# Kernel optimization log

Measured on AMD Instinct MI355X. Metric: run time of the kernel, lower is better.

Reference implementation:

```python
import jax, jax.numpy as jnp
import numpy as np

COMMITMENT_COST = 0.25
ENTROPY_LOSS_WEIGHT = 0.1
EPSILON = 1e-05
NUM_EMBEDDINGS = 2048
EMBEDDING_DIM = 64


def setup_inputs() -> dict:
    key = jax.random.key(0)
    kx, ke = jax.random.split(key)
    x = jax.random.normal(kx, (16, 64, 64, EMBEDDING_DIM), dtype=jnp.float32)
    embedding = jax.random.normal(ke, (NUM_EMBEDDINGS, EMBEDDING_DIM), dtype=jnp.float32)
    return {"x": x, "embedding": embedding}


def reference(x, embedding):
    input_shape = x.shape
    flat_x = x.reshape(-1, EMBEDDING_DIM)              # [N, D]
    distances = (jnp.sum(flat_x ** 2, axis=1, keepdims=True)
                 + jnp.sum(embedding ** 2, axis=1)
                 - 2.0 * jnp.matmul(flat_x, embedding.T))
    encoding_indices = jnp.argmin(distances, axis=1)   # [N]
    quantized = embedding[encoding_indices].reshape(input_shape)

    commitment_loss = jnp.mean((jax.lax.stop_gradient(quantized) - x) ** 2)
    codebook_loss = jnp.mean((quantized - jax.lax.stop_gradient(x)) ** 2)
    # straight-through estimator
    quantized = x + jax.lax.stop_gradient(quantized - x)

    # histogram of code usage == mean of one-hot encodings (scatter-add, avoids [N,K] one-hot)
    n_tokens = flat_x.shape[0]
    counts = jnp.zeros((NUM_EMBEDDINGS,), dtype=flat_x.dtype).at[encoding_indices].add(1.0)
    avg_probs = counts / n_tokens
    perplexity = jnp.exp(-jnp.sum(avg_probs * jnp.log(avg_probs + EPSILON)))
    entropy_loss = jnp.sum(avg_probs * jnp.log(avg_probs + EPSILON))

    vq_loss = codebook_loss + COMMITMENT_COST * commitment_loss + ENTROPY_LOSS_WEIGHT * entropy_loss
    return (quantized, vq_loss, commitment_loss, codebook_loss, perplexity,
            entropy_loss, encoding_indices.reshape(input_shape[:-1]), avg_probs)
```

## Files before the change

kernel.cpp:

```cpp
#include <hip/hip_runtime.h>
#include <float.h>

typedef _Float16 half8 __attribute__((ext_vector_type(8)));
typedef float    f32x4 __attribute__((ext_vector_type(4)));

constexpr int N_TOK = 65536;
constexpr int D     = 64;
constexpr int K     = 2048;
constexpr int TILE_C = 64;
constexpr int NTILE  = K / TILE_C;
constexpr int TOK_PER_BLK = 64;
constexpr int NBLK = N_TOK / TOK_PER_BLK;
constexpr float EPS_RESCORE = 2e-3f;

constexpr size_t QN       = (size_t)N_TOK * D;
constexpr size_t SCAL_OFF = QN;
constexpr size_t IDX_OFF  = QN + 5;
constexpr size_t PROB_OFF = IDX_OFF + N_TOK;

constexpr size_t WS_HNORM = 0;
constexpr size_t WS_COUNT = 8192;
constexpr size_t WS_BSUM  = 16384;
constexpr size_t WS_SW    = 24576;

__device__ inline unsigned long long pack_key(float d, int k) {
    unsigned u = __float_as_uint(d);
    u = (u & 0x80000000u) ? ~u : (u | 0x80000000u);
    return ((unsigned long long)u << 32) | (unsigned)k;
}

__device__ inline float unpack_dist(unsigned long long key) {
    unsigned u = (unsigned)(key >> 32);
    u = (u & 0x80000000u) ? (u & 0x7FFFFFFFu) : ~u;
    return __uint_as_float(u);
}

__device__ inline unsigned long long shfl_xor_u64_w16(unsigned long long v, int m) {
    int lo = __shfl_xor((int)(unsigned)v, m, 16);
    int hi = __shfl_xor((int)(unsigned)(v >> 32), m, 16);
    return ((unsigned long long)(unsigned)hi << 32) | (unsigned)lo;
}

__global__ __launch_bounds__(256) void vq_init(const float* __restrict__ emb,
                                               float* __restrict__ hnorm,
                                               unsigned* __restrict__ counts,
                                               double* __restrict__ blocksums,
                                               half8* __restrict__ sw) {
    const int g  = blockIdx.x * 256 + threadIdx.x;
    const int r  = g >> 3;
    const int c0 = g & 7;
    const float4* p4 = (const float4*)(emb + (size_t)r * D + 8 * c0);
    float4 q0 = p4[0], q1 = p4[1];
    float v[8] = {q0.x, q0.y, q0.z, q0.w, q1.x, q1.y, q1.z, q1.w};
    half8 h, l;
    float s = 0.f;
#pragma unroll
    for (int i = 0; i < 8; ++i) {
        s += v[i] * v[i];
        _Float16 hh = (_Float16)v[i];
        h[i] = hh;
        l[i] = (_Float16)(v[i] - (float)hh);
    }
    const int t    = r >> 6;
    const int w    = (r >> 4) & 3;
    const int m16  = r & 15;
    const int lane = (c0 & 3) * 16 + m16;
    const int slot = c0 >> 2;
    half8* dst = sw + ((size_t)((t * 4 + w) * 64 + lane)) * 4;
    dst[slot]     = h;
    dst[2 + slot] = l;

#pragma unroll
    for (int off = 1; off < 8; off <<= 1) s += __shfl_xor(s, off, 8);
    if (c0 == 0) hnorm[r] = 0.5f * s;
    if (g < K) counts[g] = 0u;
    if (g < NBLK) blocksums[g] = 0.0;
}

#define VQ_STEP(B0, B1, B2, B3, HN, CODE)                                          \
  {                                                                                \
    _Pragma("unroll")                                                              \
    for (int a = 0; a < 4; ++a) {                                                  \
      f32x4 acc = {(HN), (HN), (HN), (HN)};                                        \
      acc = __builtin_amdgcn_mfma_f32_16x16x32_f16(axh[a][0], (B0), acc, 0, 0, 0); \
      acc = __builtin_amdgcn_mfma_f32_16x16x32_f16(axh[a][1], (B1), acc, 0, 0, 0); \
      acc = __builtin_amdgcn_mfma_f32_16x16x32_f16(axl[a][0], (B0), acc, 0, 0, 0); \
      acc = __builtin_amdgcn_mfma_f32_16x16x32_f16(axl[a][1], (B1), acc, 0, 0, 0); \
      acc = __builtin_amdgcn_mfma_f32_16x16x32_f16(axh[a][0], (B2), acc, 0, 0, 0); \
      acc = __builtin_amdgcn_mfma_f32_16x16x32_f16(axh[a][1], (B3), acc, 0, 0, 0); \
      _Pragma("unroll")                                                            \
      for (int r = 0; r < 4; ++r)                                                  \
        if (acc[r] < best_d[a][r]) { best_d[a][r] = acc[r]; best_k[a][r] = (CODE); } \
    }                                                                              \
  }

__global__ __launch_bounds__(256) void vq_fused(const float* __restrict__ x,
                                                const float* __restrict__ emb,
                                                const float* __restrict__ hnorm,
                                                const half8* __restrict__ sw,
                                                unsigned* __restrict__ counts,
                                                double* __restrict__ blocksums,
                                                float* __restrict__ out) {
    __shared__ unsigned long long kls[64][5];
    __shared__ int bks[64];
    __shared__ double wsum[4];

    const int tid  = threadIdx.x;
    const int lane = tid & 63;
    const int wav  = tid >> 6;
    const int t0   = blockIdx.x * TOK_PER_BLK;
    const int m16  = lane & 15;
    const int g    = lane >> 4;
    const int ko   = g * 8;
    const int cit  = wav * 16 + m16;

    half8 axh[4][2], axl[4][2];
#pragma unroll
    for (int a = 0; a < 4; ++a) {
        const float* xr = x + (size_t)(t0 + 16 * a + m16) * D;
#pragma unroll
        for (int c = 0; c < 2; ++c) {
            const float4* p4 = (const float4*)(xr + 32 * c + ko);
            float4 q0 = p4[0], q1 = p4[1];
            float v[8] = {q0.x, q0.y, q0.z, q0.w, q1.x, q1.y, q1.z, q1.w};
            half8 h, l;
#pragma unroll
            for (int j = 0; j < 8; ++j) {
                float nv = -v[j];
                _Float16 hh = (_Float16)nv;
                h[j] = hh;
                l[j] = (_Float16)(nv - (float)hh);
            }
            axh[a][c] = h; axl[a][c] = l;
        }
    }

    float best_d[4][4];
    int   best_k[4][4];
#pragma unroll
    for (int a = 0; a < 4; ++a)
#pragma unroll
        for (int r = 0; r < 4; ++r) { best_d[a][r] = FLT_MAX; best_k[a][r] = 0; }

    const half8* pb = sw + (size_t)tid * 4;
    const float* ph = hnorm + cit;
    int code = cit;

    half8 e0 = pb[0], e1 = pb[1], e2 = pb[2], e3 = pb[3];
    float eh = *ph;

    for (int t = 0; t < NTILE; t += 2) {
        const half8* po = pb + 1024;
        half8 o0 = po[0], o1 = po[1], o2 = po[2], o3 = po[3];
        float oh = ph[64];

        VQ_STEP(e0, e1, e2, e3, eh, code);
        code += 64;

        if (t + 2 < NTILE) {
            pb += 2048; ph += 128;
            e0 = pb[0]; e1 = pb[1]; e2 = pb[2]; e3 = pb[3];
            eh = *ph;
        }

        VQ_STEP(o0, o1, o2, o3, oh, code);
        code += 64;
    }

#pragma unroll
    for (int a = 0; a < 4; ++a)
#pragma unroll
        for (int r = 0; r < 4; ++r) {
            unsigned long long key = pack_key(best_d[a][r], best_k[a][r]);
#pragma unroll
            for (int off = 8; off; off >>= 1) {
                unsigned long long o = shfl_xor_u64_w16(key, off);
                if (o < key) key = o;
            }
            if (m16 == 0) kls[16 * a + g * 4 + r][wav] = key;
        }
    __syncthreads();

    if (tid < 64) {
        float ds[4]; int kk[4];
        unsigned long long kmin = ~0ULL;
#pragma unroll
        for (int w = 0; w < 4; ++w) {
            unsigned long long key = kls[tid][w];
            ds[w] = unpack_dist(key);
            kk[w] = (int)(unsigned)(key & 0xFFFFFFFFu);
            if (key < kmin) kmin = key;
        }
        int bk = (int)(unsigned)(kmin & 0xFFFFFFFFu);
        const float fmin = unpack_dist(kmin);
        int cnt = 0;
#pragma unroll
        for (int w = 0; w < 4; ++w) cnt += (ds[w] <= fmin + EPS_RESCORE) ? 1 : 0;

        if (cnt > 1) {
            unsigned long long bkey = ~0ULL;
            const float* xr = x + (size_t)(t0 + tid) * D;
            for (int w = 0; w < 4; ++w) {
                if (ds[w] <= fmin + EPS_RESCORE) {
                    const int k = kk[w];
                    const float* cr = emb + (size_t)k * D;
                    float s0 = 0.f, s1 = 0.f, s2 = 0.f, s3 = 0.f;
#pragma unroll
                    for (int i = 0; i < 16; ++i) {
                        s0 = fmaf(cr[4 * i + 0], xr[4 * i + 0], s0);
                        s1 = fmaf(cr[4 * i + 1], xr[4 * i + 1], s1);
                        s2 = fmaf(cr[4 * i + 2], xr[4 * i + 2], s2);
                        s3 = fmaf(cr[4 * i + 3], xr[4 * i + 3], s3);
                    }
                    float hd = hnorm[k] - ((s0 + s1) + (s2 + s3));
                    unsigned long long key = pack_key(hd, k);
                    if (key < bkey) bkey = key;
                }
            }
            bk = (int)(unsigned)(bkey & 0xFFFFFFFFu);
        }
        bks[tid] = bk;
        out[IDX_OFF + t0 + tid] = (float)bk;
        atomicAdd(&counts[bk], 1u);
    }
    __syncthreads();

    const int tok = tid >> 2;
    const int i4  = tid & 3;
    const int bk  = bks[tok];
    const float4* xr4 = (const float4*)(x + (size_t)(t0 + tok) * D);
    const float4* cr4 = (const float4*)(emb + (size_t)bk * D);
    float4* qr4 = (float4*)(out + (size_t)(t0 + tok) * D);
    float local = 0.f;
#pragma unroll
    for (int ii = 0; ii < 4; ++ii) {
        const int idx = i4 + 4 * ii;
        float4 xv = xr4[idx];
        float4 cv = cr4[idx];
        float dx = cv.x - xv.x, dy = cv.y - xv.y;
        float dz = cv.z - xv.z, dw = cv.w - xv.w;
        local += dx * dx + dy * dy + dz * dz + dw * dw;
        float4 q;
        q.x = xv.x + dx; q.y = xv.y + dy;
        q.z = xv.z + dz; q.w = xv.w + dw;
        qr4[idx] = q;
    }
    double ld = (double)local;
#pragma unroll
    for (int off = 32; off > 0; off >>= 1) ld += __shfl_down(ld, off, 64);
    if (lane == 0) wsum[wav] = ld;
    __syncthreads();
    if (tid == 0)
        blocksums[blockIdx.x] = (wsum[0] + wsum[1]) + (wsum[2] + wsum[3]);
}

__global__ __launch_bounds__(256) void vq_finalize(const unsigned* __restrict__ counts,
                                                   const double* __restrict__ blocksums,
                                                   float* __restrict__ out) {
    const int tid = threadIdx.x;
    double e = 0.0;
#pragma unroll
    for (int i = 0; i < 8; ++i) {
        int k = tid + i * 256;
        float p = (float)counts[k] / 65536.0f;
        out[PROB_OFF + k] = p;
        double pd = (double)p;
        e += pd * log(pd + 1e-5);
    }
    double s = 0.0;
#pragma unroll
    for (int i = 0; i < NBLK / 256; ++i) s += blocksums[tid + i * 256];
#pragma unroll
    for (int off = 32; off > 0; off >>= 1) {
        e += __shfl_down(e, off, 64);
        s += __shfl_down(s, off, 64);
    }
    __shared__ double we[4], ws2[4];
    int lane = tid & 63, wid = tid >> 6;
    if (lane == 0) { we[wid] = e; ws2[wid] = s; }
    __syncthreads();
    if (tid == 0) {
        double entropy = (we[0] + we[1]) + (we[2] + we[3]);
        double sumsq   = (ws2[0] + ws2[1]) + (ws2[2] + ws2[3]);
        double mse     = sumsq / (double)((size_t)N_TOK * D);
        out[SCAL_OFF + 0] = (float)(1.25 * mse + 0.1 * entropy);
        out[SCAL_OFF + 1] = (float)mse;
        out[SCAL_OFF + 2] = (float)mse;
        out[SCAL_OFF + 3] = (float)exp(-entropy);
        out[SCAL_OFF + 4] = (float)entropy;
    }
}

extern "C" void kernel_launch(void* const* d_in, const int* in_sizes, int n_in,
                              void* d_out, int out_size, void* d_ws, size_t ws_size,
                              hipStream_t stream) {
    const float* x   = (const float*)d_in[0];
    const float* emb = (const float*)d_in[1];
    float* out = (float*)d_out;

    char* ws = (char*)d_ws;
    float*    hnorm     = (float*)(ws + WS_HNORM);
    unsigned* counts    = (unsigned*)(ws + WS_COUNT);
    double*   blocksums = (double*)(ws + WS_BSUM);
    half8*    sw        = (half8*)(ws + WS_SW);

    vq_init<<<K * 8 / 256, 256, 0, stream>>>(emb, hnorm, counts, blocksums, sw);
    vq_fused<<<NBLK, 256, 0, stream>>>(x, emb, hnorm, sw, counts, blocksums, out);
    vq_finalize<<<1, 256, 0, stream>>>(counts, blocksums, out);
}
```

Baseline: 134.4 us.

## Split codebook search across two blocks per token group with ticket merge

```diff
diff --git a/kernel.cpp b/kernel.cpp
--- a/kernel.cpp
+++ b/kernel.cpp
@@ -8,9 +8,10 @@
 constexpr int D     = 64;
 constexpr int K     = 2048;
 constexpr int TILE_C = 64;
-constexpr int NTILE  = K / TILE_C;
+constexpr int NTILE_H = 16;
 constexpr int TOK_PER_BLK = 64;
-constexpr int NBLK = N_TOK / TOK_PER_BLK;
+constexpr int NGRP = N_TOK / TOK_PER_BLK;
+constexpr int NBLK = NGRP * 2;
 constexpr float EPS_RESCORE = 2e-3f;
 
 constexpr size_t QN       = (size_t)N_TOK * D;
@@ -21,7 +22,9 @@
 constexpr size_t WS_HNORM = 0;
 constexpr size_t WS_COUNT = 8192;
 constexpr size_t WS_BSUM  = 16384;
-constexpr size_t WS_SW    = 24576;
+constexpr size_t WS_TICK  = 24576;
+constexpr size_t WS_KEYS  = 28672;
+constexpr size_t WS_SW    = 28672 + (size_t)2 * N_TOK * 8;
 
 __device__ inline unsigned long long pack_key(float d, int k) {
     unsigned u = __float_as_uint(d);
@@ -44,7 +47,7 @@
 __global__ __launch_bounds__(256) void vq_init(const float* __restrict__ emb,
                                                float* __restrict__ hnorm,
                                                unsigned* __restrict__ counts,
-                                               double* __restrict__ blocksums,
+                                               unsigned* __restrict__ ticket,
                                                half8* __restrict__ sw) {
     const int g  = blockIdx.x * 256 + threadIdx.x;
     const int r  = g >> 3;
@@ -66,7 +69,7 @@
     const int m16  = r & 15;
     const int lane = (c0 & 3) * 16 + m16;
     const int slot = c0 >> 2;
-    half8* dst = sw + ((size_t)((t * 4 + w) * 64 + lane)) * 4;
+    half8* dst = sw + ((size_t)(t * 256 + w * 64 + lane)) * 4;
     dst[slot]     = h;
     dst[2 + slot] = l;
 
@@ -74,7 +77,7 @@
     for (int off = 1; off < 8; off <<= 1) s += __shfl_xor(s, off, 8);
     if (c0 == 0) hnorm[r] = 0.5f * s;
     if (g < K) counts[g] = 0u;
-    if (g < NBLK) blocksums[g] = 0.0;
+    if (g < NGRP) ticket[g] = 0u;
 }
 
 #define VQ_STEP(B0, B1, B2, B3, HN, CODE)                                          \
@@ -99,20 +102,26 @@
                                                 const float* __restrict__ hnorm,
                                                 const half8* __restrict__ sw,
                                                 unsigned* __restrict__ counts,
+                                                unsigned* __restrict__ ticket,
+                                                unsigned long long* __restrict__ keys,
                                                 double* __restrict__ blocksums,
                                                 float* __restrict__ out) {
     __shared__ unsigned long long kls[64][5];
     __shared__ int bks[64];
     __shared__ double wsum[4];
+    __shared__ int is_last_s;
 
     const int tid  = threadIdx.x;
     const int lane = tid & 63;
     const int wav  = tid >> 6;
-    const int t0   = blockIdx.x * TOK_PER_BLK;
+    const int grp  = blockIdx.x >> 1;
+    const int half = blockIdx.x & 1;
+    const int t0   = grp * TOK_PER_BLK;
     const int m16  = lane & 15;
     const int g    = lane >> 4;
     const int ko   = g * 8;
     const int cit  = wav * 16 + m16;
+    const int cbase = half * (K / 2);
 
     half8 axh[4][2], axl[4][2];
 #pragma unroll
@@ -142,14 +151,14 @@
 #pragma unroll
         for (int r = 0; r < 4; ++r) { best_d[a][r] = FLT_MAX; best_k[a][r] = 0; }
 
-    const half8* pb = sw + (size_t)tid * 4;
-    const float* ph = hnorm + cit;
-    int code = cit;
+    const half8* pb = sw + ((size_t)(half * NTILE_H) * 256 + tid) * 4;
+    const float* ph = hnorm + cbase + cit;
+    int code = cbase + cit;
 
     half8 e0 = pb[0], e1 = pb[1], e2 = pb[2], e3 = pb[3];
     float eh = *ph;
 
-    for (int t = 0; t < NTILE; t += 2) {
+    for (int t = 0; t < NTILE_H; t += 2) {
         const half8* po = pb + 1024;
         half8 o0 = po[0], o1 = po[1], o2 = po[2], o3 = po[3];
         float oh = ph[64];
@@ -157,7 +166,7 @@
         VQ_STEP(e0, e1, e2, e3, eh, code);
         code += 64;
 
-        if (t + 2 < NTILE) {
+        if (t + 2 < NTILE_H) {
             pb += 2048; ph += 128;
             e0 = pb[0]; e1 = pb[1]; e2 = pb[2]; e3 = pb[3];
             eh = *ph;
@@ -191,7 +200,6 @@
             kk[w] = (int)(unsigned)(key & 0xFFFFFFFFu);
             if (key < kmin) kmin = key;
         }
-        int bk = (int)(unsigned)(kmin & 0xFFFFFFFFu);
         const float fmin = unpack_dist(kmin);
         int cnt = 0;
 #pragma unroll
@@ -217,10 +225,52 @@
                     if (key < bkey) bkey = key;
                 }
             }
+            kmin = bkey;
+        }
+        keys[(size_t)half * N_TOK + t0 + tid] = kmin;
+        __threadfence();
+    }
+    __syncthreads();
+    if (tid == 0)
+        is_last_s = (atomicAdd(&ticket[grp], 1u) == 1u);
+    __syncthreads();
+    if (!is_last_s) return;
+    __threadfence();
+
+    if (tid < 64) {
+        const int tok = t0 + tid;
+        unsigned long long k0 = keys[tok];
+        unsigned long long k1 = keys[(size_t)N_TOK + tok];
+        float d0 = unpack_dist(k0), d1 = unpack_dist(k1);
+        unsigned long long kmin = (k0 < k1) ? k0 : k1;
+        int bk = (int)(unsigned)(kmin & 0xFFFFFFFFu);
+        const float fmin = unpack_dist(kmin);
+
+        if (d0 <= fmin + EPS_RESCORE && d1 <= fmin + EPS_RESCORE) {
+            unsigned long long bkey = ~0ULL;
+            const float* xr = x + (size_t)tok * D;
+            const int cand[2] = {(int)(unsigned)(k0 & 0xFFFFFFFFu),
+                                 (int)(unsigned)(k1 & 0xFFFFFFFFu)};
+#pragma unroll
+            for (int w = 0; w < 2; ++w) {
+                const int k = cand[w];
+                const float* cr = emb + (size_t)k * D;
+                float s0 = 0.f, s1 = 0.f, s2 = 0.f, s3 = 0.f;
+#pragma unroll
+                for (int i = 0; i < 16; ++i) {
+                    s0 = fmaf(cr[4 * i + 0], xr[4 * i + 0], s0);
+                    s1 = fmaf(cr[4 * i + 1], xr[4 * i + 1], s1);
+                    s2 = fmaf(cr[4 * i + 2], xr[4 * i + 2], s2);
+                    s3 = fmaf(cr[4 * i + 3], xr[4 * i + 3], s3);
+                }
+                float hd = hnorm[k] - ((s0 + s1) + (s2 + s3));
+                unsigned long long key = pack_key(hd, k);
+                if (key < bkey) bkey = key;
+            }
             bk = (int)(unsigned)(bkey & 0xFFFFFFFFu);
         }
         bks[tid] = bk;
-        out[IDX_OFF + t0 + tid] = (float)bk;
+        out[IDX_OFF + tok] = (float)bk;
         atomicAdd(&counts[bk], 1u);
     }
     __syncthreads();
@@ -251,7 +301,7 @@
     if (lane == 0) wsum[wav] = ld;
     __syncthreads();
     if (tid == 0)
-        blocksums[blockIdx.x] = (wsum[0] + wsum[1]) + (wsum[2] + wsum[3]);
+        blocksums[grp] = (wsum[0] + wsum[1]) + (wsum[2] + wsum[3]);
 }
 
 __global__ __launch_bounds__(256) void vq_finalize(const unsigned* __restrict__ counts,
@@ -269,7 +319,7 @@
     }
     double s = 0.0;
 #pragma unroll
-    for (int i = 0; i < NBLK / 256; ++i) s += blocksums[tid + i * 256];
+    for (int i = 0; i < NGRP / 256; ++i) s += blocksums[tid + i * 256];
 #pragma unroll
     for (int off = 32; off > 0; off >>= 1) {
         e += __shfl_down(e, off, 64);
@@ -302,9 +352,12 @@
     float*    hnorm     = (float*)(ws + WS_HNORM);
     unsigned* counts    = (unsigned*)(ws + WS_COUNT);
     double*   blocksums = (double*)(ws + WS_BSUM);
+    unsigned* ticket    = (unsigned*)(ws + WS_TICK);
+    unsigned long long* keys = (unsigned long long*)(ws + WS_KEYS);
     half8*    sw        = (half8*)(ws + WS_SW);
 
-    vq_init<<<K * 8 / 256, 256, 0, stream>>>(emb, hnorm, counts, blocksums, sw);
-    vq_fused<<<NBLK, 256, 0, stream>>>(x, emb, hnorm, sw, counts, blocksums, out);
+    vq_init<<<K * 8 / 256, 256, 0, stream>>>(emb, hnorm, counts, ticket, sw);
+    vq_fused<<<NBLK, 256, 0, stream>>>(x, emb, hnorm, sw, counts, ticket, keys,
+                                       blocksums, out);
     vq_finalize<<<1, 256, 0, stream>>>(counts, blocksums, out);
 }
```

Result: slower. 360.4 us (+168.1%).

## Deepen codebook prefetch to two tiles ahead and batch MFMAs under raised priority

Applied to the files above, without the earlier changes.

```diff
diff --git a/kernel.cpp b/kernel.cpp
--- a/kernel.cpp
+++ b/kernel.cpp
@@ -66,7 +66,7 @@
     const int m16  = r & 15;
     const int lane = (c0 & 3) * 16 + m16;
     const int slot = c0 >> 2;
-    half8* dst = sw + ((size_t)((t * 4 + w) * 64 + lane)) * 4;
+    half8* dst = sw + ((size_t)(t * 256 + w * 64 + lane)) * 4;
     dst[slot]     = h;
     dst[2 + slot] = l;
 
@@ -77,30 +77,42 @@
     if (g < NBLK) blocksums[g] = 0.0;
 }
 
-#define VQ_STEP(B0, B1, B2, B3, HN, CODE)                                          \
+#define LOADB(TOFF, B, HN)                                                         \
   {                                                                                \
+    const half8* _q = pb + (TOFF) * 1024;                                          \
+    B##0 = _q[0]; B##1 = _q[1]; B##2 = _q[2]; B##3 = _q[3];                        \
+    HN = ph[(TOFF) * 64];                                                          \
+  }
+
+#define VQ_STEP(B, HN, CODE)                                                       \
+  {                                                                                \
+    f32x4 acc[4];                                                                  \
+    __builtin_amdgcn_s_setprio(1);                                                 \
     _Pragma("unroll")                                                              \
     for (int a = 0; a < 4; ++a) {                                                  \
-      f32x4 acc = {(HN), (HN), (HN), (HN)};                                        \
-      acc = __builtin_amdgcn_mfma_f32_16x16x32_f16(axh[a][0], (B0), acc, 0, 0, 0); \
-      acc = __builtin_amdgcn_mfma_f32_16x16x32_f16(axh[a][1], (B1), acc, 0, 0, 0); \
-      acc = __builtin_amdgcn_mfma_f32_16x16x32_f16(axl[a][0], (B0), acc, 0, 0, 0); \
-      acc = __builtin_amdgcn_mfma_f32_16x16x32_f16(axl[a][1], (B1), acc, 0, 0, 0); \
-      acc = __builtin_amdgcn_mfma_f32_16x16x32_f16(axh[a][0], (B2), acc, 0, 0, 0); \
-      acc = __builtin_amdgcn_mfma_f32_16x16x32_f16(axh[a][1], (B3), acc, 0, 0, 0); \
+      acc[a] = (f32x4){(HN), (HN), (HN), (HN)};                                    \
+      acc[a] = __builtin_amdgcn_mfma_f32_16x16x32_f16(axh[a][0], B##0, acc[a], 0, 0, 0); \
+      acc[a] = __builtin_amdgcn_mfma_f32_16x16x32_f16(axh[a][1], B##1, acc[a], 0, 0, 0); \
+      acc[a] = __builtin_amdgcn_mfma_f32_16x16x32_f16(axl[a][0], B##0, acc[a], 0, 0, 0); \
+      acc[a] = __builtin_amdgcn_mfma_f32_16x16x32_f16(axl[a][1], B##1, acc[a], 0, 0, 0); \
+      acc[a] = __builtin_amdgcn_mfma_f32_16x16x32_f16(axh[a][0], B##2, acc[a], 0, 0, 0); \
+      acc[a] = __builtin_amdgcn_mfma_f32_16x16x32_f16(axh[a][1], B##3, acc[a], 0, 0, 0); \
+    }                                                                              \
+    __builtin_amdgcn_s_setprio(0);                                                 \
+    _Pragma("unroll")                                                              \
+    for (int a = 0; a < 4; ++a)                                                    \
       _Pragma("unroll")                                                            \
       for (int r = 0; r < 4; ++r)                                                  \
-        if (acc[r] < best_d[a][r]) { best_d[a][r] = acc[r]; best_k[a][r] = (CODE); } \
-    }                                                                              \
+        if (acc[a][r] < best_d[a][r]) { best_d[a][r] = acc[a][r]; best_k[a][r] = (CODE); } \
   }
 
-__global__ __launch_bounds__(256) void vq_fused(const float* __restrict__ x,
-                                                const float* __restrict__ emb,
-                                                const float* __restrict__ hnorm,
-                                                const half8* __restrict__ sw,
-                                                unsigned* __restrict__ counts,
-                                                double* __restrict__ blocksums,
-                                                float* __restrict__ out) {
+__global__ __launch_bounds__(256, 4) void vq_fused(const float* __restrict__ x,
+                                                   const float* __restrict__ emb,
+                                                   const float* __restrict__ hnorm,
+                                                   const half8* __restrict__ sw,
+                                                   unsigned* __restrict__ counts,
+                                                   double* __restrict__ blocksums,
+                                                   float* __restrict__ out) {
     __shared__ unsigned long long kls[64][5];
     __shared__ int bks[64];
     __shared__ double wsum[4];
@@ -146,25 +158,24 @@
     const float* ph = hnorm + cit;
     int code = cit;
 
-    half8 e0 = pb[0], e1 = pb[1], e2 = pb[2], e3 = pb[3];
-    float eh = *ph;
-
-    for (int t = 0; t < NTILE; t += 2) {
-        const half8* po = pb + 1024;
-        half8 o0 = po[0], o1 = po[1], o2 = po[2], o3 = po[3];
-        float oh = ph[64];
-
-        VQ_STEP(e0, e1, e2, e3, eh, code);
-        code += 64;
-
-        if (t + 2 < NTILE) {
-            pb += 2048; ph += 128;
-            e0 = pb[0]; e1 = pb[1]; e2 = pb[2]; e3 = pb[3];
-            eh = *ph;
-        }
-
-        VQ_STEP(o0, o1, o2, o3, oh, code);
-        code += 64;
+    half8 b00, b01, b02, b03;  float h0;
+    half8 b10, b11, b12, b13;  float h1;
+    half8 b20, b21, b22, b23;  float h2;
+    half8 b30, b31, b32, b33;  float h3;
+
+    LOADB(0, b0, h0);
+    LOADB(1, b1, h1);
+
+    for (int t = 0; t < NTILE; t += 4) {
+        if (t + 2 < NTILE) LOADB(2, b2, h2);
+        VQ_STEP(b0, h0, code);              code += 64;
+        if (t + 3 < NTILE) LOADB(3, b3, h3);
+        VQ_STEP(b1, h1, code);              code += 64;
+        if (t + 4 < NTILE) LOADB(4, b0, h0);
+        VQ_STEP(b2, h2, code);              code += 64;
+        if (t + 5 < NTILE) LOADB(5, b1, h1);
+        VQ_STEP(b3, h3, code);              code += 64;
+        pb += 4096; ph += 256;
     }
 
 #pragma unroll
```

Result: slower. 494.5 us (+267.9%).

## Switch to 32x32x16 MFMA with tile index packed into distance low bits

Applied to the files above, without the earlier changes.

```diff
diff --git a/kernel.cpp b/kernel.cpp
--- a/kernel.cpp
+++ b/kernel.cpp
@@ -2,7 +2,8 @@
 #include <float.h>
 
 typedef _Float16 half8 __attribute__((ext_vector_type(8)));
-typedef float    f32x4 __attribute__((ext_vector_type(4)));
+typedef float    f32x4  __attribute__((ext_vector_type(4)));
+typedef float    f32x16 __attribute__((ext_vector_type(16)));
 
 constexpr int N_TOK = 65536;
 constexpr int D     = 64;
@@ -35,9 +36,9 @@
     return __uint_as_float(u);
 }
 
-__device__ inline unsigned long long shfl_xor_u64_w16(unsigned long long v, int m) {
-    int lo = __shfl_xor((int)(unsigned)v, m, 16);
-    int hi = __shfl_xor((int)(unsigned)(v >> 32), m, 16);
+__device__ inline unsigned long long shfl_xor_u64_w32(unsigned long long v, int m) {
+    int lo = __shfl_xor((int)(unsigned)v, m, 32);
+    int hi = __shfl_xor((int)(unsigned)(v >> 32), m, 32);
     return ((unsigned long long)(unsigned)hi << 32) | (unsigned)lo;
 }
 
@@ -62,13 +63,12 @@
         l[i] = (_Float16)(v[i] - (float)hh);
     }
     const int t    = r >> 6;
-    const int w    = (r >> 4) & 3;
-    const int m16  = r & 15;
-    const int lane = (c0 & 3) * 16 + m16;
-    const int slot = c0 >> 2;
-    half8* dst = sw + ((size_t)((t * 4 + w) * 64 + lane)) * 4;
-    dst[slot]     = h;
-    dst[2 + slot] = l;
+    const int ct   = (r >> 5) & 1;
+    const int lane = (c0 & 1) * 32 + (r & 31);
+    const int f    = c0 >> 1;
+    half8* dst = sw + ((size_t)((t * 2 + ct) * 64 + lane)) * 8;
+    dst[f]     = h;
+    dst[4 + f] = l;
 
 #pragma unroll
     for (int off = 1; off < 8; off <<= 1) s += __shfl_xor(s, off, 8);
@@ -77,20 +77,37 @@
     if (g < NBLK) blocksums[g] = 0.0;
 }
 
-#define VQ_STEP(B0, B1, B2, B3, HN, CODE)                                          \
+#define LOADB(TOFF, H0, H1, H2, H3, L0, L1, L2, L3, HN)                            \
   {                                                                                \
+    const half8* _q = pb + (TOFF) * 1024;                                          \
+    H0 = _q[0]; H1 = _q[1]; H2 = _q[2]; H3 = _q[3];                                \
+    L0 = _q[4]; L1 = _q[5]; L2 = _q[6]; L3 = _q[7];                                \
+    HN = ph[(TOFF) * 64];                                                          \
+  }
+
+#define VQ_STEP(H0, H1, H2, H3, L0, L1, L2, L3, HN, TT)                            \
+  {                                                                                \
+    f32x16 acc;                                                                    \
     _Pragma("unroll")                                                              \
-    for (int a = 0; a < 4; ++a) {                                                  \
-      f32x4 acc = {(HN), (HN), (HN), (HN)};                                        \
-      acc = __builtin_amdgcn_mfma_f32_16x16x32_f16(axh[a][0], (B0), acc, 0, 0, 0); \
-      acc = __builtin_amdgcn_mfma_f32_16x16x32_f16(axh[a][1], (B1), acc, 0, 0, 0); \
-      acc = __builtin_amdgcn_mfma_f32_16x16x32_f16(axl[a][0], (B0), acc, 0, 0, 0); \
-      acc = __builtin_amdgcn_mfma_f32_16x16x32_f16(axl[a][1], (B1), acc, 0, 0, 0); \
-      acc = __builtin_amdgcn_mfma_f32_16x16x32_f16(axh[a][0], (B2), acc, 0, 0, 0); \
-      acc = __builtin_amdgcn_mfma_f32_16x16x32_f16(axh[a][1], (B3), acc, 0, 0, 0); \
-      _Pragma("unroll")                                                            \
-      for (int r = 0; r < 4; ++r)                                                  \
-        if (acc[r] < best_d[a][r]) { best_d[a][r] = acc[r]; best_k[a][r] = (CODE); } \
+    for (int i = 0; i < 16; ++i) acc[i] = (HN);                                    \
+    __builtin_amdgcn_s_setprio(1);                                                 \
+    acc = __builtin_amdgcn_mfma_f32_32x32x16_f16(axh[0], H0, acc, 0, 0, 0);        \
+    acc = __builtin_amdgcn_mfma_f32_32x32x16_f16(axh[1], H1, acc, 0, 0, 0);        \
+    acc = __builtin_amdgcn_mfma_f32_32x32x16_f16(axh[2], H2, acc, 0, 0, 0);        \
+    acc = __builtin_amdgcn_mfma_f32_32x32x16_f16(axh[3], H3, acc, 0, 0, 0);        \
+    acc = __builtin_amdgcn_mfma_f32_32x32x16_f16(axl[0], H0, acc, 0, 0, 0);        \
+    acc = __builtin_amdgcn_mfma_f32_32x32x16_f16(axl[1], H1, acc, 0, 0, 0);        \
+    acc = __builtin_amdgcn_mfma_f32_32x32x16_f16(axl[2], H2, acc, 0, 0, 0);        \
+    acc = __builtin_amdgcn_mfma_f32_32x32x16_f16(axl[3], H3, acc, 0, 0, 0);        \
+    acc = __builtin_amdgcn_mfma_f32_32x32x16_f16(axh[0], L0, acc, 0, 0, 0);        \
+    acc = __builtin_amdgcn_mfma_f32_32x32x16_f16(axh[1], L1, acc, 0, 0, 0);        \
+    acc = __builtin_amdgcn_mfma_f32_32x32x16_f16(axh[2], L2, acc, 0, 0, 0);        \
+    acc = __builtin_amdgcn_mfma_f32_32x32x16_f16(axh[3], L3, acc, 0, 0, 0);        \
+    __builtin_amdgcn_s_setprio(0);                                                 \
+    _Pragma("unroll")                                                              \
+    for (int i = 0; i < 16; ++i) {                                                 \
+      unsigned _kb = (__float_as_uint(acc[i]) & 0xFFFFFFE0u) | (unsigned)(TT);     \
+      best_d[i] = fminf(best_d[i], __uint_as_float(_kb));                          \
     }                                                                              \
   }
 
@@ -101,7 +118,7 @@
                                                 unsigned* __restrict__ counts,
                                                 double* __restrict__ blocksums,
                                                 float* __restrict__ out) {
-    __shared__ unsigned long long kls[64][5];
+    __shared__ unsigned long long kls[64][3];
     __shared__ int bks[64];
     __shared__ double wsum[4];
 
@@ -109,18 +126,17 @@
     const int lane = tid & 63;
     const int wav  = tid >> 6;
     const int t0   = blockIdx.x * TOK_PER_BLK;
-    const int m16  = lane & 15;
-    const int g    = lane >> 4;
-    const int ko   = g * 8;
-    const int cit  = wav * 16 + m16;
-
-    half8 axh[4][2], axl[4][2];
-#pragma unroll
-    for (int a = 0; a < 4; ++a) {
-        const float* xr = x + (size_t)(t0 + 16 * a + m16) * D;
-#pragma unroll
-        for (int c = 0; c < 2; ++c) {
-            const float4* p4 = (const float4*)(xr + 32 * c + ko);
+    const int col  = lane & 31;
+    const int h5   = lane >> 5;
+    const int tt   = wav >> 1;
+    const int ct   = wav & 1;
+
+    half8 axh[4], axl[4];
+    {
+        const float* xr = x + (size_t)(t0 + tt * 32 + col) * D + h5 * 8;
+#pragma unroll
+        for (int kk = 0; kk < 4; ++kk) {
+            const float4* p4 = (const float4*)(xr + kk * 16);
             float4 q0 = p4[0], q1 = p4[1];
             float v[8] = {q0.x, q0.y, q0.z, q0.w, q1.x, q1.y, q1.z, q1.w};
             half8 h, l;
@@ -131,91 +147,76 @@
                 h[j] = hh;
                 l[j] = (_Float16)(nv - (float)hh);
             }
-            axh[a][c] = h; axl[a][c] = l;
+            axh[kk] = h; axl[kk] = l;
         }
     }
 
-    float best_d[4][4];
-    int   best_k[4][4];
-#pragma unroll
-    for (int a = 0; a < 4; ++a)
-#pragma unroll
-        for (int r = 0; r < 4; ++r) { best_d[a][r] = FLT_MAX; best_k[a][r] = 0; }
-
-    const half8* pb = sw + (size_t)tid * 4;
-    const float* ph = hnorm + cit;
-    int code = cit;
-
-    half8 e0 = pb[0], e1 = pb[1], e2 = pb[2], e3 = pb[3];
-    float eh = *ph;
+    float best_d[16];
+#pragma unroll
+    for (int i = 0; i < 16; ++i) best_d[i] = FLT_MAX;
+
+    const half8* pb = sw + (size_t)(ct * 64 + lane) * 8;
+    const float* ph = hnorm + ct * 32 + col;
+
+    half8 eH0, eH1, eH2, eH3, eL0, eL1, eL2, eL3;  float hE;
+    half8 oH0, oH1, oH2, oH3, oL0, oL1, oL2, oL3;  float hO;
+
+    LOADB(0, eH0, eH1, eH2, eH3, eL0, eL1, eL2, eL3, hE);
 
     for (int t = 0; t < NTILE; t += 2) {
-        const half8* po = pb + 1024;
-        half8 o0 = po[0], o1 = po[1], o2 = po[2], o3 = po[3];
-        float oh = ph[64];
-
-        VQ_STEP(e0, e1, e2, e3, eh, code);
-        code += 64;
-
-        if (t + 2 < NTILE) {
-            pb += 2048; ph += 128;
-            e0 = pb[0]; e1 = pb[1]; e2 = pb[2]; e3 = pb[3];
-            eh = *ph;
+        LOADB(1, oH0, oH1, oH2, oH3, oL0, oL1, oL2, oL3, hO);
+        VQ_STEP(eH0, eH1, eH2, eH3, eL0, eL1, eL2, eL3, hE, t);
+        if (t + 2 < NTILE)
+            LOADB(2, eH0, eH1, eH2, eH3, eL0, eL1, eL2, eL3, hE);
+        VQ_STEP(oH0, oH1, oH2, oH3, oL0, oL1, oL2, oL3, hO, t + 1);
+        pb += 2048; ph += 128;
+    }
+
+#pragma unroll
+    for (int reg = 0; reg < 16; ++reg) {
+        const unsigned bits = __float_as_uint(best_d[reg]);
+        const int code = (int)(bits & 31u) * TILE_C + ct * 32 + col;
+        unsigned long long key = pack_key(best_d[reg], code);
+#pragma unroll
+        for (int off = 16; off; off >>= 1) {
+            unsigned long long o = shfl_xor_u64_w32(key, off);
+            if (o < key) key = o;
         }
-
-        VQ_STEP(o0, o1, o2, o3, oh, code);
-        code += 64;
-    }
-
-#pragma unroll
-    for (int a = 0; a < 4; ++a)
-#pragma unroll
-        for (int r = 0; r < 4; ++r) {
-            unsigned long long key = pack_key(best_d[a][r], best_k[a][r]);
-#pragma unroll
-            for (int off = 8; off; off >>= 1) {
-                unsigned long long o = shfl_xor_u64_w16(key, off);
-                if (o < key) key = o;
-            }
-            if (m16 == 0) kls[16 * a + g * 4 + r][wav] = key;
+        if (col == 0) {
+            const int tl = tt * 32 + (reg & 3) + 8 * (reg >> 2) + 4 * h5;
+            kls[tl][ct] = key;
         }
+    }
     __syncthreads();
 
     if (tid < 64) {
-        float ds[4]; int kk[4];
-        unsigned long long kmin = ~0ULL;
-#pragma unroll
-        for (int w = 0; w < 4; ++w) {
-            unsigned long long key = kls[tid][w];
-            ds[w] = unpack_dist(key);
-            kk[w] = (int)(unsigned)(key & 0xFFFFFFFFu);
-            if (key < kmin) kmin = key;
-        }
+        unsigned long long k0 = kls[tid][0];
+        unsigned long long k1 = kls[tid][1];
+        const float d0 = unpack_dist(k0), d1 = unpack_dist(k1);
+        unsigned long long kmin = (k0 < k1) ? k0 : k1;
         int bk = (int)(unsigned)(kmin & 0xFFFFFFFFu);
         const float fmin = unpack_dist(kmin);
-        int cnt = 0;
-#pragma unroll
-        for (int w = 0; w < 4; ++w) cnt += (ds[w] <= fmin + EPS_RESCORE) ? 1 : 0;
-
-        if (cnt > 1) {
+
+        if (d0 <= fmin + EPS_RESCORE && d1 <= fmin + EPS_RESCORE) {
             unsigned long long bkey = ~0ULL;
             const float* xr = x + (size_t)(t0 + tid) * D;
-            for (int w = 0; w < 4; ++w) {
-                if (ds[w] <= fmin + EPS_RESCORE) {
-                    const int k = kk[w];
-                    const float* cr = emb + (size_t)k * D;
-                    float s0 = 0.f, s1 = 0.f, s2 = 0.f, s3 = 0.f;
-#pragma unroll
-                    for (int i = 0; i < 16; ++i) {
-                        s0 = fmaf(cr[4 * i + 0], xr[4 * i + 0], s0);
-                        s1 = fmaf(cr[4 * i + 1], xr[4 * i + 1], s1);
-                        s2 = fmaf(cr[4 * i + 2], xr[4 * i + 2], s2);
-                        s3 = fmaf(cr[4 * i + 3], xr[4 * i + 3], s3);
-                    }
-                    float hd = hnorm[k] - ((s0 + s1) + (s2 + s3));
-                    unsigned long long key = pack_key(hd, k);
-                    if (key < bkey) bkey = key;
+            const int cand[2] = {(int)(unsigned)(k0 & 0xFFFFFFFFu),
+                                 (int)(unsigned)(k1 & 0xFFFFFFFFu)};
+#pragma unroll
+            for (int w = 0; w < 2; ++w) {
+                const int k = cand[w];
+                const float* cr = emb + (size_t)k * D;
+                float s0 = 0.f, s1 = 0.f, s2 = 0.f, s3 = 0.f;
+#pragma unroll
+                for (int i = 0; i < 16; ++i) {
+                    s0 = fmaf(cr[4 * i + 0], xr[4 * i + 0], s0);
+                    s1 = fmaf(cr[4 * i + 1], xr[4 * i + 1], s1);
+                    s2 = fmaf(cr[4 * i + 2], xr[4 * i + 2], s2);
+                    s3 = fmaf(cr[4 * i + 3], xr[4 * i + 3], s3);
                 }
+                float hd = hnorm[k] - ((s0 + s1) + (s2 + s3));
+                unsigned long long key = pack_key(hd, k);
+                if (key < bkey) bkey = key;
             }
             bk = (int)(unsigned)(bkey & 0xFFFFFFFFu);
         }
```

New measurement: 199.3 us. +48.3%, slower.
